# Kernel optimization log

Measured on AMD Instinct MI355X. Metric: run time of the kernel, lower is better.

Reference implementation:

```python
import jax, jax.numpy as jnp
import numpy as np

B, L, D, W = 4, 512, 768, 12
K = L * W  # number of candidate spans


def _mlp(x, w1, b1, w2, b2):
    # Linear -> ReLU -> (Dropout=identity in eval) -> Linear
    return jax.nn.relu(x @ w1.T + b1) @ w2.T + b2


def setup_inputs() -> dict:
    key = jax.random.key(0)
    ks = jax.random.split(key, 16)
    sc_d = 1.0 / np.sqrt(D)
    sc_4d = 1.0 / np.sqrt(4 * D)
    sc_2d = 1.0 / np.sqrt(2 * D)
    inp = {
        "h": jax.random.normal(ks[0], (B, L, D), dtype=jnp.float32),
        "span_idx": jax.random.randint(ks[1], (B, K, 2), 0, L, dtype=jnp.int64),
        # project_start: Linear(D,4D), Linear(4D,D)
        "ws1": jax.random.uniform(ks[2], (4 * D, D), jnp.float32, -sc_d, sc_d),
        "bs1": jax.random.uniform(ks[3], (4 * D,), jnp.float32, -sc_d, sc_d),
        "ws2": jax.random.uniform(ks[4], (D, 4 * D), jnp.float32, -sc_4d, sc_4d),
        "bs2": jax.random.uniform(ks[5], (D,), jnp.float32, -sc_4d, sc_4d),
        # project_end
        "we1": jax.random.uniform(ks[6], (4 * D, D), jnp.float32, -sc_d, sc_d),
        "be1": jax.random.uniform(ks[7], (4 * D,), jnp.float32, -sc_d, sc_d),
        "we2": jax.random.uniform(ks[8], (D, 4 * D), jnp.float32, -sc_4d, sc_4d),
        "be2": jax.random.uniform(ks[9], (D,), jnp.float32, -sc_4d, sc_4d),
        # out_project: Linear(2D,4D), Linear(4D,D)
        "wo1": jax.random.uniform(ks[10], (4 * D, 2 * D), jnp.float32, -sc_2d, sc_2d),
        "bo1": jax.random.uniform(ks[11], (4 * D,), jnp.float32, -sc_2d, sc_2d),
        "wo2": jax.random.uniform(ks[12], (D, 4 * D), jnp.float32, -sc_4d, sc_4d),
        "bo2": jax.random.uniform(ks[13], (D,), jnp.float32, -sc_4d, sc_4d),
    }
    return inp


def reference(h, span_idx, ws1, bs1, ws2, bs2, we1, be1, we2, be2, wo1, bo1, wo2, bo2):
    start_rep = _mlp(h, ws1, bs1, ws2, bs2)  # [B, L, D]
    end_rep = _mlp(h, we1, be1, we2, be2)    # [B, L, D]
    bidx = jnp.arange(B)[:, None]
    start_span = start_rep[bidx, span_idx[:, :, 0]]  # gather along seq dim -> [B, K, D]
    end_span = end_rep[bidx, span_idx[:, :, 1]]      # [B, K, D]
    cat = jax.nn.relu(jnp.concatenate([start_span, end_span], axis=-1))  # [B, K, 2D]
    out = _mlp(cat, wo1, bo1, wo2, bo2)  # [B, K, D]
    return out.reshape(B, L, W, D)
```

## Files before the change

kernel.cpp:

```cpp
#include <hip/hip_runtime.h>
#include <hip/hip_bf16.h>

using bf16 = __hip_bfloat16;
using bf16x8 = __attribute__((ext_vector_type(8))) __bf16;
using f32x4  = __attribute__((ext_vector_type(4))) float;
typedef unsigned short ushort_t;

#define BM 128
#define BN 128
#define BK 32


__device__ __forceinline__ void gl_lds16(const void* g, void* l) {
  __builtin_amdgcn_global_load_lds(
      (const __attribute__((address_space(1))) void*)g,
      (__attribute__((address_space(3))) void*)l, 16, 0, 0);
}

__device__ __forceinline__ ushort_t f2bf(float f) {
  unsigned u = __float_as_uint(f);
  u += 0x7FFF + ((u >> 16) & 1);
  return (ushort_t)(u >> 16);
}

__global__ void sniff(const unsigned* __restrict__ w1,
                      const unsigned* __restrict__ idx, int* flags) {
  __shared__ int cnt[2];
  if (threadIdx.x == 0) { cnt[0] = 0; cnt[1] = 0; }
  __syncthreads();
  int t = threadIdx.x;
  int c0 = 0;
  for (int k = 0; k < 4; ++k) {
    unsigned lo = w1[t * 4 + k] & 0xFFFFu;
    unsigned e = (lo >> 7) & 0xFF;
    if (e <= 122) c0++;
  }
  int c1 = (idx[2 * t + 1] != 0) ? 1 : 0;
  atomicAdd(&cnt[0], c0);
  atomicAdd(&cnt[1], c1);
  __syncthreads();
  if (threadIdx.x == 0) {
    flags[0] = (cnt[0] >= 900) ? 1 : 0;
    flags[1] = (cnt[1] == 0) ? 1 : 0;
  }
}

__global__ void norm_idx(const int* __restrict__ flags, const void* __restrict__ src,
                         int* __restrict__ dst) {
  int i = blockIdx.x * 256 + threadIdx.x;
  int v = flags[1] ? (int)((const long long*)src)[i] : ((const int*)src)[i];
  dst[i] = v;
}

__global__ void cvt_all(const int* __restrict__ flags,
                        const void* s0, const void* s1, const void* s2,
                        const void* s3, const void* s4, const void* s5,
                        const void* s6, ushort_t* __restrict__ dst) {
  long i = ((long)blockIdx.x * 256 + threadIdx.x) * 4;
  const void* src; long off;
  if      (i <  1572864) { src = s0; off = i; }
  else if (i <  3932160) { src = s1; off = i - 1572864; }
  else if (i <  6291456) { src = s2; off = i - 3932160; }
  else if (i <  8650752) { src = s3; off = i - 6291456; }
  else if (i < 11010048) { src = s4; off = i - 8650752; }
  else if (i < 15728640) { src = s5; off = i - 11010048; }
  else                   { src = s6; off = i - 15728640; }
  if (flags[0]) {
    *(ushort4*)(dst + i) = *((const ushort4*)((const ushort_t*)src + off));
  } else {
    float4 f = ((const float4*)src)[off >> 2];
    ushort4 o;
    o.x = f2bf(f.x); o.y = f2bf(f.y); o.z = f2bf(f.z); o.w = f2bf(f.w);
    *(ushort4*)(dst + i) = o;
  }
}

__global__ void cvt_bias(const int* __restrict__ flags,
                         const void* b0, const void* b1, const void* b2,
                         const void* b3, const void* b4, const void* b5,
                         float* __restrict__ dst) {
  int i = blockIdx.x * 256 + threadIdx.x;
  if (i >= 14592) return;
  if (i >= 11520) { dst[i] = 0.f; return; }
  const void* src; int off;
  if (i < 3072)       { src = b0; off = i; }
  else if (i < 3840)  { src = b1; off = i - 3072; }
  else if (i < 6912)  { src = b2; off = i - 3840; }
  else if (i < 7680)  { src = b3; off = i - 6912; }
  else if (i < 10752) { src = b4; off = i - 7680; }
  else                { src = b5; off = i - 10752; }
  dst[i] = flags[0] ? __bfloat162float(((const bf16*)src)[off])
                    : ((const float*)src)[off];
}

template <bool GATHER, bool RELU, bool OUTF32>
__global__ __launch_bounds__(256) void gemm_bt(
    const bf16* __restrict__ A, const bf16* __restrict__ A2,
    const bf16* __restrict__ repS, const bf16* __restrict__ repE,
    const int* __restrict__ sidx, int row_base,
    const bf16* __restrict__ Bw, const bf16* __restrict__ Bw2,
    const float* __restrict__ bias, const float* __restrict__ bias2,
    void* __restrict__ C, void* __restrict__ C2, int nsplit,
    int N, int Kdim, int bstride) {
  __shared__ bf16 lA[BM * BK];
  __shared__ bf16 lB[BN * BK];

  const int tid  = threadIdx.x;
  const int lane = tid & 63;
  const int wave = tid >> 6;
  const int wm = wave >> 1, wn = wave & 1;
  int by = blockIdx.y;
  const bf16* Bw_ = Bw; const float* bias_ = bias; void* C_ = C; const bf16* A_ = A;
  if (by >= nsplit) { by -= nsplit; Bw_ = Bw2; bias_ = bias2; C_ = C2; A_ = A2; }
  const int m0 = blockIdx.x * BM;
  const int n0 = by * BN;

  const int srow = tid >> 2;
  const int scol = 8 * ((tid & 3) ^ ((tid >> 3) & 3));

  const bf16 *a0 = nullptr, *a1 = nullptr;
  const bf16 *pS0 = nullptr, *pE0 = nullptr, *pS1 = nullptr, *pE1 = nullptr;
  if (GATHER) {
    int r0 = row_base + m0 + srow;
    int r1 = r0 + 64;
    int b0 = r0 / 6144, b1 = r1 / 6144;
    int s0 = min(max(sidx[2 * r0], 0), 511);
    int e0 = min(max(sidx[2 * r0 + 1], 0), 511);
    int s1 = min(max(sidx[2 * r1], 0), 511);
    int e1 = min(max(sidx[2 * r1 + 1], 0), 511);
    pS0 = repS + ((size_t)b0 * 512 + s0) * 768 + scol;
    pE0 = repE + ((size_t)b0 * 512 + e0) * 768 + scol;
    pS1 = repS + ((size_t)b1 * 512 + s1) * 768 + scol;
    pE1 = repE + ((size_t)b1 * 512 + e1) * 768 + scol;
  } else {
    a0 = A_ + (size_t)(m0 + srow) * Kdim + scol;
    a1 = a0 + (size_t)64 * Kdim;
  }
  const bf16* b0p = Bw_ + (size_t)(n0 + srow) * bstride + scol;
  const bf16* b1p = b0p + (size_t)64 * bstride;

  f32x4 acc[4][4];
  const f32x4 z = {0.f, 0.f, 0.f, 0.f};
#pragma unroll
  for (int i = 0; i < 4; ++i)
#pragma unroll
    for (int j = 0; j < 4; ++j) acc[i][j] = z;

  const int fr = lane & 15;
  const int fk = 8 * ((lane >> 4) ^ ((lane >> 1) & 3));

  for (int k0 = 0; k0 < Kdim; k0 += BK) {
    const bf16 *sa0, *sa1;
    if (GATHER) {
      if (k0 < 768) { sa0 = pS0 + k0; sa1 = pS1 + k0; }
      else          { sa0 = pE0 + (k0 - 768); sa1 = pE1 + (k0 - 768); }
    } else {
      sa0 = a0 + k0; sa1 = a1 + k0;
    }
    gl_lds16(sa0, lA + tid * 8);
    gl_lds16(sa1, lA + 2048 + tid * 8);
    gl_lds16(b0p + k0, lB + tid * 8);
    gl_lds16(b1p + k0, lB + 2048 + tid * 8);
    __syncthreads();

    bf16x8 af[4], bv[4];
#pragma unroll
    for (int i = 0; i < 4; ++i)
      af[i] = *(const bf16x8*)(const void*)(lA + (wm * 64 + i * 16 + fr) * BK + fk);
#pragma unroll
    for (int j = 0; j < 4; ++j)
      bv[j] = *(const bf16x8*)(const void*)(lB + (wn * 64 + j * 16 + fr) * BK + fk);
#pragma unroll
    for (int i = 0; i < 4; ++i)
#pragma unroll
      for (int j = 0; j < 4; ++j)
        acc[i][j] = __builtin_amdgcn_mfma_f32_16x16x32_bf16(af[i], bv[j], acc[i][j], 0, 0, 0);
    __syncthreads();
  }

  float* Cf = (float*)C_;
  bf16*  Cb = (bf16*)C_;
#pragma unroll
  for (int j = 0; j < 4; ++j) {
    int n = n0 + wn * 64 + j * 16 + fr;
    float bj = bias_[n];
#pragma unroll
    for (int i = 0; i < 4; ++i) {
      int mb = m0 + wm * 64 + i * 16 + (lane >> 4) * 4;
#pragma unroll
      for (int r = 0; r < 4; ++r) {
        float v = acc[i][j][r] + bj;
        if (RELU) v = fmaxf(v, 0.f);
        if (OUTF32) Cf[(size_t)(mb + r) * N + n] = v;
        else        Cb[(size_t)(mb + r) * N + n] = __float2bfloat16(v);
      }
    }
  }
}

__global__ __launch_bounds__(256) void gemm_final_fused(
    const ushort_t* __restrict__ Ps, const ushort_t* __restrict__ Pe,
    const int* __restrict__ sidx,
    const bf16* __restrict__ Bw, const float* __restrict__ bias,
    float* __restrict__ out) {
  __shared__ bf16 lA[BM * BK];
  __shared__ bf16 lB[BN * BK];

  const int tid  = threadIdx.x;
  const int lane = tid & 63;
  const int wave = tid >> 6;
  const int wm = wave >> 1, wn = wave & 1;
  const int m0 = blockIdx.x * BM;
  const int n0 = blockIdx.y * BN;

  const int srow = tid >> 2;
  const int scol = 8 * ((tid & 3) ^ ((tid >> 3) & 3));

  int r0 = m0 + srow, r1 = r0 + 64;
  int b0 = r0 / 6144, b1 = r1 / 6144;
  int s0 = min(max(sidx[2 * r0], 0), 511);
  int e0 = min(max(sidx[2 * r0 + 1], 0), 511);
  int s1 = min(max(sidx[2 * r1], 0), 511);
  int e1 = min(max(sidx[2 * r1 + 1], 0), 511);
  const ushort_t* pS0 = Ps + ((size_t)b0 * 512 + s0) * 3072 + scol;
  const ushort_t* pE0 = Pe + ((size_t)b0 * 512 + e0) * 3072 + scol;
  const ushort_t* pS1 = Ps + ((size_t)b1 * 512 + s1) * 3072 + scol;
  const ushort_t* pE1 = Pe + ((size_t)b1 * 512 + e1) * 3072 + scol;

  const bf16* bp0 = Bw + (size_t)(n0 + srow) * 3072 + scol;
  const bf16* bp1 = bp0 + (size_t)64 * 3072;

  f32x4 acc[4][4];
  const f32x4 z = {0.f, 0.f, 0.f, 0.f};
#pragma unroll
  for (int i = 0; i < 4; ++i)
#pragma unroll
    for (int j = 0; j < 4; ++j) acc[i][j] = z;

  const int fr = lane & 15;
  const int fk = 8 * ((lane >> 4) ^ ((lane >> 1) & 3));

  for (int k0 = 0; k0 < 3072; k0 += BK) {
    gl_lds16(bp0 + k0, lB + tid * 8);
    gl_lds16(bp1 + k0, lB + 2048 + tid * 8);
#pragma unroll
    for (int h = 0; h < 2; ++h) {
      uint4 xs = *(const uint4*)(const void*)((h ? pS1 : pS0) + k0);
      uint4 xe = *(const uint4*)(const void*)((h ? pE1 : pE0) + k0);
      unsigned w[4];
      const unsigned* us = &xs.x;
      const unsigned* ue = &xe.x;
#pragma unroll
      for (int q = 0; q < 4; ++q) {
        float lo = __uint_as_float(us[q] << 16) + __uint_as_float(ue[q] << 16);
        float hi = __uint_as_float(us[q] & 0xFFFF0000u) +
                   __uint_as_float(ue[q] & 0xFFFF0000u);
        w[q] = (unsigned)f2bf(fmaxf(lo, 0.f)) |
               ((unsigned)f2bf(fmaxf(hi, 0.f)) << 16);
      }
      *(uint4*)(void*)(lA + h * 2048 + tid * 8) = *(const uint4*)w;
    }
    __syncthreads();

    bf16x8 af[4], bv[4];
#pragma unroll
    for (int i = 0; i < 4; ++i)
      af[i] = *(const bf16x8*)(const void*)(lA + (wm * 64 + i * 16 + fr) * BK + fk);
#pragma unroll
    for (int j = 0; j < 4; ++j)
      bv[j] = *(const bf16x8*)(const void*)(lB + (wn * 64 + j * 16 + fr) * BK + fk);
#pragma unroll
    for (int i = 0; i < 4; ++i)
#pragma unroll
      for (int j = 0; j < 4; ++j)
        acc[i][j] = __builtin_amdgcn_mfma_f32_16x16x32_bf16(af[i], bv[j], acc[i][j], 0, 0, 0);
    __syncthreads();
  }

#pragma unroll
  for (int j = 0; j < 4; ++j) {
    int n = n0 + wn * 64 + j * 16 + fr;
    float bj = bias[n];
#pragma unroll
    for (int i = 0; i < 4; ++i) {
      int mb = m0 + wm * 64 + i * 16 + (lane >> 4) * 4;
#pragma unroll
      for (int r = 0; r < 4; ++r)
        out[(size_t)(mb + r) * 768 + n] = acc[i][j][r] + bj;
    }
  }
}

extern "C" void kernel_launch(void* const* d_in, const int* in_sizes, int n_in,
                              void* d_out, int out_size, void* d_ws, size_t ws_size,
                              hipStream_t stream) {
  const void* h    = d_in[0];
  const void* sidx = d_in[1];
  const void *ws1 = d_in[2],  *bs1 = d_in[3];
  const void *ws2 = d_in[4],  *bs2 = d_in[5];
  const void *we1 = d_in[6],  *be1 = d_in[7];
  const void *we2 = d_in[8],  *be2 = d_in[9];
  const void *wo1 = d_in[10], *bo1 = d_in[11];
  const void *wo2 = d_in[12], *bo2 = d_in[13];

  char* p = (char*)d_ws;
  int*      flags = (int*)p;
  int*      idx32 = (int*)(p + 256);
  float*    biasf = (float*)(p + 256 + 196608);
  ushort_t* hb    = (ushort_t*)(p + 256 + 196608 + 65536);
  ushort_t* w1sb  = hb   + (size_t)1572864;
  ushort_t* w2sb  = w1sb + (size_t)2359296;
  ushort_t* w1eb  = w2sb + (size_t)2359296;
  ushort_t* w2eb  = w1eb + (size_t)2359296;
  ushort_t* wo1b  = w2eb + (size_t)2359296;
  ushort_t* wo2b  = wo1b + (size_t)4718592;
  ushort_t* repS  = wo2b + (size_t)2359296;
  ushort_t* repE  = repS + (size_t)1572864;
  char*     R     = (char*)(repE + (size_t)1572864);
  size_t fixed = (size_t)(R - (char*)d_ws);
  if (ws_size < fixed) return;
  size_t Rsz = ws_size - fixed;

  const size_t P_BF = (size_t)2 * 2048 * 3072 * 2;
  int tier = (Rsz >= P_BF) ? 2 : 3;

  dim3 blk(256);
  const int XBIG = 0x40000000;
  sniff<<<1, blk, 0, stream>>>((const unsigned*)ws1, (const unsigned*)sidx, flags);
  norm_idx<<<192, blk, 0, stream>>>(flags, sidx, idx32);
  cvt_all<<<17664, blk, 0, stream>>>(flags, h, ws1, ws2, we1, we2, wo1, wo2, hb);
  cvt_bias<<<57, blk, 0, stream>>>(flags, bs1, bs2, be1, be2, bo1, bo2, biasf);
  const float *bs1f = biasf, *bs2f = biasf + 3072, *be1f = biasf + 3840,
              *be2f = biasf + 6912, *bo1f = biasf + 7680, *bo2f = biasf + 10752,
              *zerof = biasf + 11520;
  float* outf = (float*)d_out;

  if (tier == 2) {
    ushort_t* hidS = (ushort_t*)R;
    ushort_t* hidE = hidS + (size_t)2048 * 3072;
    gemm_bt<false, true, false><<<dim3(16, 48), blk, 0, stream>>>(
        (const bf16*)hb, (const bf16*)hb, nullptr, nullptr, nullptr, 0,
        (const bf16*)w1sb, (const bf16*)w1eb, bs1f, be1f,
        hidS, hidE, 24, 3072, 768, 768);
    gemm_bt<false, true, false><<<dim3(16, 12), blk, 0, stream>>>(
        (const bf16*)hidS, (const bf16*)hidE, nullptr, nullptr, nullptr, 0,
        (const bf16*)w2sb, (const bf16*)w2eb, bs2f, be2f,
        (bf16*)repS, (bf16*)repE, 6, 768, 3072, 3072);
    ushort_t* Ps = (ushort_t*)R;
    ushort_t* Pe = Ps + (size_t)2048 * 3072;
    gemm_bt<false, false, false><<<dim3(16, 48), blk, 0, stream>>>(
        (const bf16*)repS, (const bf16*)repE, nullptr, nullptr, nullptr, 0,
        (const bf16*)wo1b, (const bf16*)wo1b + 768, bo1f, zerof,
        Ps, Pe, 24, 3072, 768, 1536);
    gemm_final_fused<<<dim3(192, 6), blk, 0, stream>>>(
        Ps, Pe, idx32, (const bf16*)wo2b, bo2f, outf);
  } else {
    long long cT = (long long)(Rsz / ((size_t)2 * 3072 * 2));
    cT = (cT / 128) * 128; if (cT > 2048) cT = 2048;
    long long cO = (long long)(Rsz / ((size_t)3072 * 2));
    cO = (cO / 128) * 128; if (cO > 24576) cO = 24576;
    if (cT < 128 || cO < 128) return;
    ushort_t* scr = (ushort_t*)R;
    for (long long r = 0; r < 2048; r += cT) {
      long long mc = 2048 - r < cT ? 2048 - r : cT;
      ushort_t* hidS = scr;
      ushort_t* hidE = scr + (size_t)cT * 3072;
      gemm_bt<false, true, false><<<dim3(mc / 128, 48), blk, 0, stream>>>(
          (const bf16*)hb + r * 768, (const bf16*)hb + r * 768,
          nullptr, nullptr, nullptr, 0,
          (const bf16*)w1sb, (const bf16*)w1eb, bs1f, be1f,
          hidS, hidE, 24, 3072, 768, 768);
      gemm_bt<false, true, false><<<dim3(mc / 128, 12), blk, 0, stream>>>(
          (const bf16*)hidS, (const bf16*)hidE, nullptr, nullptr, nullptr, 0,
          (const bf16*)w2sb, (const bf16*)w2eb, bs2f, be2f,
          (bf16*)repS + r * 768, (bf16*)repE + r * 768, 6, 768, 3072, 3072);
    }
    for (long long r = 0; r < 24576; r += cO) {
      long long mc = 24576 - r < cO ? 24576 - r : cO;
      gemm_bt<true, true, false><<<dim3(mc / 128, 24), blk, 0, stream>>>(
          nullptr, nullptr, (const bf16*)repS, (const bf16*)repE, idx32, (int)r,
          (const bf16*)wo1b, nullptr, bo1f, nullptr,
          scr, nullptr, XBIG, 3072, 1536, 1536);
      gemm_bt<false, false, true><<<dim3(mc / 128, 6), blk, 0, stream>>>(
          (const bf16*)scr, nullptr, nullptr, nullptr, nullptr, 0,
          (const bf16*)wo2b, nullptr, bo2f, nullptr,
          outf + (size_t)r * 768, nullptr, XBIG, 768, 3072, 3072);
    }
  }
}
```

Before: 585.4 us.

## Double-buffer LDS in fused gather GEMM to overlap loads with MFMA

Converts the final fused gather+GEMM kernel from single-buffered LDS with two barriers per K-step to a double-buffered pipeline with one barrier per step. The next tile's weight loads (global_load_lds) and gathered activation loads are issued before the current tile's MFMAs, and the pack/ReLU/store to LDS happens after them. This hides global memory latency behind compute. The cost is twice the LDS use and more live registers for the prefetched vectors, which may lower occupancy.

```diff
diff --git a/kernel.cpp b/kernel.cpp
--- a/kernel.cpp
+++ b/kernel.cpp
@@ -203,8 +203,8 @@
     const int* __restrict__ sidx,
     const bf16* __restrict__ Bw, const float* __restrict__ bias,
     float* __restrict__ out) {
-  __shared__ bf16 lA[BM * BK];
-  __shared__ bf16 lB[BN * BK];
+  __shared__ bf16 lA[2 * 4096];
+  __shared__ bf16 lB[2 * 4096];
 
   const int tid  = threadIdx.x;
   const int lane = tid & 63;
@@ -240,40 +240,65 @@
   const int fr = lane & 15;
   const int fk = 8 * ((lane >> 4) ^ ((lane >> 1) & 3));
 
-  for (int k0 = 0; k0 < 3072; k0 += BK) {
-    gl_lds16(bp0 + k0, lB + tid * 8);
-    gl_lds16(bp1 + k0, lB + 2048 + tid * 8);
-#pragma unroll
-    for (int h = 0; h < 2; ++h) {
-      uint4 xs = *(const uint4*)(const void*)((h ? pS1 : pS0) + k0);
-      uint4 xe = *(const uint4*)(const void*)((h ? pE1 : pE0) + k0);
-      unsigned w[4];
-      const unsigned* us = &xs.x;
-      const unsigned* ue = &xe.x;
-#pragma unroll
-      for (int q = 0; q < 4; ++q) {
-        float lo = __uint_as_float(us[q] << 16) + __uint_as_float(ue[q] << 16);
-        float hi = __uint_as_float(us[q] & 0xFFFF0000u) +
-                   __uint_as_float(ue[q] & 0xFFFF0000u);
-        w[q] = (unsigned)f2bf(fmaxf(lo, 0.f)) |
-               ((unsigned)f2bf(fmaxf(hi, 0.f)) << 16);
-      }
-      *(uint4*)(void*)(lA + h * 2048 + tid * 8) = *(const uint4*)w;
-    }
+  auto pack_store = [&](uint4 xs, uint4 xe, bf16* dst) {
+    unsigned w[4];
+    const unsigned* us = &xs.x;
+    const unsigned* ue = &xe.x;
+#pragma unroll
+    for (int q = 0; q < 4; ++q) {
+      float lo = __uint_as_float(us[q] << 16) + __uint_as_float(ue[q] << 16);
+      float hi = __uint_as_float(us[q] & 0xFFFF0000u) +
+                 __uint_as_float(ue[q] & 0xFFFF0000u);
+      w[q] = (unsigned)f2bf(fmaxf(lo, 0.f)) |
+             ((unsigned)f2bf(fmaxf(hi, 0.f)) << 16);
+    }
+    *(uint4*)(void*)dst = *(const uint4*)w;
+  };
+
+  {
+    gl_lds16(bp0, lB + tid * 8);
+    gl_lds16(bp1, lB + 2048 + tid * 8);
+    uint4 xs0 = *(const uint4*)(const void*)pS0;
+    uint4 xe0 = *(const uint4*)(const void*)pE0;
+    uint4 xs1 = *(const uint4*)(const void*)pS1;
+    uint4 xe1 = *(const uint4*)(const void*)pE1;
+    pack_store(xs0, xe0, lA + tid * 8);
+    pack_store(xs1, xe1, lA + 2048 + tid * 8);
     __syncthreads();
+  }
+
+  for (int it = 0; it < 96; ++it) {
+    const int cur = (it & 1) << 12;
+    const int nxt = ((it + 1) & 1) << 12;
+    const int k1 = (it + 1) * BK;
+    const bool pre = (it + 1) < 96;
+    uint4 xs0, xe0, xs1, xe1;
+    if (pre) {
+      gl_lds16(bp0 + k1, lB + nxt + tid * 8);
+      gl_lds16(bp1 + k1, lB + nxt + 2048 + tid * 8);
+      xs0 = *(const uint4*)(const void*)(pS0 + k1);
+      xe0 = *(const uint4*)(const void*)(pE0 + k1);
+      xs1 = *(const uint4*)(const void*)(pS1 + k1);
+      xe1 = *(const uint4*)(const void*)(pE1 + k1);
+    }
 
     bf16x8 af[4], bv[4];
 #pragma unroll
     for (int i = 0; i < 4; ++i)
-      af[i] = *(const bf16x8*)(const void*)(lA + (wm * 64 + i * 16 + fr) * BK + fk);
+      af[i] = *(const bf16x8*)(const void*)(lA + cur + (wm * 64 + i * 16 + fr) * BK + fk);
 #pragma unroll
     for (int j = 0; j < 4; ++j)
-      bv[j] = *(const bf16x8*)(const void*)(lB + (wn * 64 + j * 16 + fr) * BK + fk);
+      bv[j] = *(const bf16x8*)(const void*)(lB + cur + (wn * 64 + j * 16 + fr) * BK + fk);
 #pragma unroll
     for (int i = 0; i < 4; ++i)
 #pragma unroll
       for (int j = 0; j < 4; ++j)
         acc[i][j] = __builtin_amdgcn_mfma_f32_16x16x32_bf16(af[i], bv[j], acc[i][j], 0, 0, 0);
+
+    if (pre) {
+      pack_store(xs0, xe0, lA + nxt + tid * 8);
+      pack_store(xs1, xe1, lA + nxt + 2048 + tid * 8);
+    }
     __syncthreads();
   }
 
```

Result: faster. 558.8 us (-4.5%).
